# Optimization experiments

Measured on AMD Instinct MI355X. Metric: run time of the kernel, lower is better.

Reference implementation:

```python
import jax, jax.numpy as jnp
import numpy as np

HUGE = 1e31  # ops.HUGE_INT
EPS = 1e-20

NUM_ENT, NUM_REL = 100000, 400
ENT_D, REL_D, HIST_D = 256, 256, 512
ACT_D = ENT_D + REL_D          # 512
IN_D = ENT_D + HIST_D + REL_D  # 1024
B, A = 512, 256


def setup_inputs() -> dict:
    key = jax.random.key(0)
    ks = jax.random.split(key, 10)
    s = 0.02
    return {
        "current_entity": jax.random.randint(ks[0], (B,), 0, NUM_ENT),
        "query_relation": jax.random.randint(ks[1], (B,), 0, NUM_REL),
        "encoded_history": jax.random.normal(ks[2], (B, HIST_D), jnp.float32),
        "r_space": jax.random.randint(ks[3], (B, A), 0, NUM_REL),
        "e_space": jax.random.randint(ks[4], (B, A), 0, NUM_ENT),
        "action_mask": jax.random.randint(ks[5], (B, A), 0, 2).astype(jnp.int32),
        "entity_emb": jax.random.normal(ks[6], (NUM_ENT, ENT_D), jnp.float32) * s,
        "relation_emb": jax.random.normal(ks[7], (NUM_REL, REL_D), jnp.float32) * s,
        "W1": jax.random.normal(ks[8], (IN_D, ACT_D), jnp.float32) * s,
        "b1": jnp.zeros((ACT_D,), jnp.float32),
        "W2": jax.random.normal(ks[9], (ACT_D, ACT_D), jnp.float32) * s,
        "b2": jnp.zeros((ACT_D,), jnp.float32),
    }


def reference(current_entity, query_relation, encoded_history, r_space, e_space,
              action_mask, entity_emb, relation_emb, W1, b1, W2, b2):
    # encode_history: [E(cur) | lstm hidden | R(query)] -> [B, IN_D]
    X = jnp.concatenate([entity_emb[current_entity], encoded_history,
                         relation_emb[query_relation]], axis=-1)
    # policy MLP (dropout = identity in eval)
    X2 = jax.nn.relu(X @ W1 + b1) @ W2 + b2          # [B, ACT_D]
    # per-action embeddings: concat(rel, ent) -> [B, A, ACT_D]
    A_emb = jnp.concatenate([relation_emb[r_space], entity_emb[e_space]], axis=-1)
    mask = action_mask.astype(X2.dtype)
    scores = jnp.einsum('bad,bd->ba', A_emb, X2) - (1.0 - mask) * HUGE
    action_dist = jax.nn.softmax(scores, axis=-1)    # [B, A]
    entropy = -jnp.sum(action_dist * jnp.log(action_dist + EPS), axis=-1)  # [B]
    return action_dist, entropy
```

## Files before the change

### kernel.cpp

```cpp
#include <hip/hip_runtime.h>
#include <hip/hip_bf16.h>

#define ENT_D 256
#define REL_D 256
#define HIST_D 512
#define ACT_DD 512
#define IN_DD 1024
#define BB 512
#define AA 256

typedef short bf16x8 __attribute__((ext_vector_type(8)));
typedef float floatx4 __attribute__((ext_vector_type(4)));

__device__ __forceinline__ unsigned short f2bf(float f) {
    unsigned u = __builtin_bit_cast(unsigned, f);
    return (unsigned short)((u + 0x7fffu + ((u >> 16) & 1u)) >> 16);
}


__global__ __launch_bounds__(256) void pack_kernel(
    const int* __restrict__ cur, const int* __restrict__ qrel,
    const float* __restrict__ hist,
    const float* __restrict__ ent_emb, const float* __restrict__ rel_emb,
    const float* __restrict__ W1, const float* __restrict__ W2,
    unsigned short* __restrict__ W1p, unsigned short* __restrict__ W2p,
    unsigned short* __restrict__ Xp)
{
    const int wid  = blockIdx.x * 4 + (threadIdx.x >> 6);
    const int lane = threadIdx.x & 63;
    const int l15  = lane & 15;
    const int quad = lane >> 4;
    unsigned short v[8];

    if (wid < 1024) {
        const int t = wid, nt = t >> 5, kt = t & 31;
        const int n = nt * 16 + l15, k0 = kt * 32 + quad * 8;
#pragma unroll
        for (int j = 0; j < 8; ++j) v[j] = f2bf(W1[(size_t)(k0 + j) * ACT_DD + n]);
        *(bf16x8*)(W1p + ((size_t)t * 64 + lane) * 8) = *(bf16x8*)v;
    } else if (wid < 1536) {
        const int t = wid - 1024, nt = t >> 4, kt = t & 15;
        const int n = nt * 16 + l15, k0 = kt * 32 + quad * 8;
#pragma unroll
        for (int j = 0; j < 8; ++j) v[j] = f2bf(W2[(size_t)(k0 + j) * ACT_DD + n]);
        *(bf16x8*)(W2p + ((size_t)t * 64 + lane) * 8) = *(bf16x8*)v;
    } else {
        const int t = wid - 1536, mt = t >> 5, kt = t & 31;
        const int m = mt * 16 + l15, k0 = kt * 32 + quad * 8;
        const float* src;
        if (k0 < ENT_D)            src = ent_emb + (size_t)cur[m] * ENT_D + k0;
        else if (k0 < ENT_D + HIST_D) src = hist + (size_t)m * HIST_D + (k0 - ENT_D);
        else                       src = rel_emb + (size_t)qrel[m] * REL_D + (k0 - ENT_D - HIST_D);
        float4 a = *(const float4*)src, b = *(const float4*)(src + 4);
        v[0]=f2bf(a.x); v[1]=f2bf(a.y); v[2]=f2bf(a.z); v[3]=f2bf(a.w);
        v[4]=f2bf(b.x); v[5]=f2bf(b.y); v[6]=f2bf(b.z); v[7]=f2bf(b.w);
        *(bf16x8*)(Xp + ((size_t)t * 64 + lane) * 8) = *(bf16x8*)v;
    }
}

__global__ __launch_bounds__(256) void gemm1_kernel(
    const unsigned short* __restrict__ Xp, const unsigned short* __restrict__ W1p,
    const float* __restrict__ b1, unsigned short* __restrict__ Hp)
{
    __shared__ unsigned short sH[1024];
    const int mt = blockIdx.x, wave = threadIdx.x >> 6, lane = threadIdx.x & 63;
    const int nt = blockIdx.y * 4 + wave;

    const bf16x8* Av = (const bf16x8*)Xp  + (size_t)mt * 32 * 64 + lane;
    const bf16x8* Bv = (const bf16x8*)W1p + (size_t)nt * 32 * 64 + lane;
    floatx4 acc = {0.f, 0.f, 0.f, 0.f};
#pragma unroll 8
    for (int kt = 0; kt < 32; ++kt)
        acc = __builtin_amdgcn_mfma_f32_16x16x32_bf16(Av[kt * 64], Bv[kt * 64], acc, 0, 0, 0);

    const int col  = nt * 16 + (lane & 15);
    const float bj = b1[col];
    const int n_loc = wave * 16 + (lane & 15);
    const int tile_loc = n_loc >> 5, quad2 = (n_loc & 31) >> 3, j2 = n_loc & 7;
#pragma unroll
    for (int reg = 0; reg < 4; ++reg) {
        const int row = (lane >> 4) * 4 + reg;
        const float h = fmaxf(acc[reg] + bj, 0.f);
        sH[tile_loc * 512 + (row + 16 * quad2) * 8 + j2] = f2bf(h);
    }
    __syncthreads();
    const int h = threadIdx.x * 4;
    const int tl = h >> 9, rest = h & 511;
    const size_t dst = ((size_t)(mt * 16 + blockIdx.y * 2 + tl) * 512 + rest);
    *(uint2*)(Hp + dst) = *(const uint2*)(sH + h);
}

__global__ __launch_bounds__(256) void gemm2_kernel(
    const unsigned short* __restrict__ Hp, const unsigned short* __restrict__ W2p,
    const float* __restrict__ b2, float* __restrict__ X2)
{
    const int mt = blockIdx.x, wave = threadIdx.x >> 6, lane = threadIdx.x & 63;
    const int nt = blockIdx.y * 4 + wave;

    const bf16x8* Av = (const bf16x8*)Hp  + (size_t)mt * 16 * 64 + lane;
    const bf16x8* Bv = (const bf16x8*)W2p + (size_t)nt * 16 * 64 + lane;
    floatx4 acc = {0.f, 0.f, 0.f, 0.f};
#pragma unroll
    for (int kt = 0; kt < 16; ++kt)
        acc = __builtin_amdgcn_mfma_f32_16x16x32_bf16(Av[kt * 64], Bv[kt * 64], acc, 0, 0, 0);

    const int col = nt * 16 + (lane & 15);
    const float bj = b2[col];
#pragma unroll
    for (int reg = 0; reg < 4; ++reg) {
        const int m = mt * 16 + (lane >> 4) * 4 + reg;
        X2[(size_t)m * ACT_DD + col] = acc[reg] + bj;
    }
}

__global__ __launch_bounds__(512) void score_softmax_kernel(
    const float* __restrict__ X2,
    const int* __restrict__ r_space, const int* __restrict__ e_space,
    const int* __restrict__ amask,
    const float* __restrict__ ent_emb, const float* __restrict__ rel_emb,
    float* __restrict__ dist, float* __restrict__ ent_out)
{
    __shared__ __align__(16) float x2s[ACT_DD];
    __shared__ float sc[AA];
    __shared__ float red[8];

    const int b = blockIdx.x, tid = threadIdx.x;
    const int wave = tid >> 6, lane = tid & 63;

    x2s[tid] = X2[(size_t)b * ACT_DD + tid];
    __syncthreads();

    const float4 xr = ((const float4*)&x2s[0])[lane];
    const float4 xe = ((const float4*)&x2s[REL_D])[lane];

#pragma unroll
    for (int g = 0; g < 4; ++g) {
        const int ab = wave * 32 + g * 8;
        int ir[8], ie[8];
#pragma unroll
        for (int i = 0; i < 8; ++i) {
            ir[i] = r_space[b * AA + ab + i];
            ie[i] = e_space[b * AA + ab + i];
        }
        float4 r4[8], e4[8];
#pragma unroll
        for (int i = 0; i < 8; ++i)
            r4[i] = ((const float4*)(rel_emb + (size_t)ir[i] * REL_D))[lane];
#pragma unroll
        for (int i = 0; i < 8; ++i)
            e4[i] = ((const float4*)(ent_emb + (size_t)ie[i] * ENT_D))[lane];

        float p[8];
#pragma unroll
        for (int i = 0; i < 8; ++i)
            p[i] = r4[i].x * xr.x + r4[i].y * xr.y + r4[i].z * xr.z + r4[i].w * xr.w
                 + e4[i].x * xe.x + e4[i].y * xe.y + e4[i].z * xe.z + e4[i].w * xe.w;
#pragma unroll
        for (int off = 32; off > 0; off >>= 1) {
#pragma unroll
            for (int i = 0; i < 8; ++i) p[i] += __shfl_xor(p[i], off, 64);
        }
        if (lane == 0) {
#pragma unroll
            for (int i = 0; i < 8; ++i) sc[ab + i] = p[i];
        }
    }
    __syncthreads();

    float s = -3.0e38f;
    if (tid < AA) {
        const float m = (float)amask[b * AA + tid];
        s = sc[tid] - (1.0f - m) * 1e31f;
    }
    float v = s;
#pragma unroll
    for (int off = 32; off > 0; off >>= 1) v = fmaxf(v, __shfl_xor(v, off, 64));
    if (lane == 0) red[wave] = v;
    __syncthreads();
    float mx = red[0];
#pragma unroll
    for (int w = 1; w < 8; ++w) mx = fmaxf(mx, red[w]);
    __syncthreads();

    const float e = (tid < AA) ? __expf(s - mx) : 0.0f;
    v = e;
#pragma unroll
    for (int off = 32; off > 0; off >>= 1) v += __shfl_xor(v, off, 64);
    if (lane == 0) red[wave] = v;
    __syncthreads();
    float sum = red[0];
#pragma unroll
    for (int w = 1; w < 8; ++w) sum += red[w];
    __syncthreads();

    const float p = e / sum;
    if (tid < AA) dist[(size_t)b * AA + tid] = p;

    v = (tid < AA) ? p * __logf(p + 1e-20f) : 0.0f;
#pragma unroll
    for (int off = 32; off > 0; off >>= 1) v += __shfl_xor(v, off, 64);
    if (lane == 0) red[wave] = v;
    __syncthreads();
    if (tid == 0) {
        float t = red[0];
#pragma unroll
        for (int w = 1; w < 8; ++w) t += red[w];
        ent_out[b] = -t;
    }
}

extern "C" void kernel_launch(void* const* d_in, const int* in_sizes, int n_in,
                              void* d_out, int out_size, void* d_ws, size_t ws_size,
                              hipStream_t stream) {
    const int*   cur      = (const int*)d_in[0];
    const int*   qrel     = (const int*)d_in[1];
    const float* hist     = (const float*)d_in[2];
    const int*   r_space  = (const int*)d_in[3];
    const int*   e_space  = (const int*)d_in[4];
    const int*   amask    = (const int*)d_in[5];
    const float* ent_emb  = (const float*)d_in[6];
    const float* rel_emb  = (const float*)d_in[7];
    const float* W1       = (const float*)d_in[8];
    const float* b1       = (const float*)d_in[9];
    const float* W2       = (const float*)d_in[10];
    const float* b2       = (const float*)d_in[11];

    float* dist    = (float*)d_out;
    float* entropy = dist + (size_t)BB * AA;

    char* w = (char*)d_ws;
    unsigned short* W1p = (unsigned short*)(w);
    unsigned short* W2p = (unsigned short*)(w + (1u << 20));
    unsigned short* Xp  = (unsigned short*)(w + (3u << 19));
    unsigned short* Hp  = (unsigned short*)(w + (5u << 19));
    float*          X2  = (float*)(w + (6u << 19));

    pack_kernel<<<640, 256, 0, stream>>>(cur, qrel, hist, ent_emb, rel_emb, W1, W2, W1p, W2p, Xp);
    gemm1_kernel<<<dim3(32, 8), 256, 0, stream>>>(Xp, W1p, b1, Hp);
    gemm2_kernel<<<dim3(32, 8), 256, 0, stream>>>(Hp, W2p, b2, X2);
    score_softmax_kernel<<<512, 512, 0, stream>>>(X2, r_space, e_space, amask,
                                                  ent_emb, rel_emb, dist, entropy);
}
```

Measured before the change: 189.6 us.

## Compact unmasked actions and gather embeddings only for valid actions

Result: faster. 184.8 us (-2.6%).

```diff
diff --git a/kernel.cpp b/kernel.cpp
--- a/kernel.cpp
+++ b/kernel.cpp
@@ -122,25 +122,55 @@
 {
     __shared__ __align__(16) float x2s[ACT_DD];
     __shared__ float sc[AA];
+    __shared__ int   list[AA];
+    __shared__ int   wcnt[4];
+    __shared__ int   n_u_s;
     __shared__ float red[8];
 
     const int b = blockIdx.x, tid = threadIdx.x;
     const int wave = tid >> 6, lane = tid & 63;
 
     x2s[tid] = X2[(size_t)b * ACT_DD + tid];
+
+    int m = 0;
+    unsigned long long bal = 0;
+    int pre = 0;
+    if (tid < AA) {
+        m = amask[b * AA + tid];
+        sc[tid] = 0.0f;
+    }
+    if (wave < 4) {
+        bal = __ballot(m != 0);
+        pre = __popcll(bal & ((1ull << lane) - 1ull));
+        if (lane == 0) wcnt[wave] = __popcll(bal);
+    }
+    __syncthreads();
+
+    if (wave < 4) {
+        int off = 0;
+#pragma unroll
+        for (int w = 0; w < 4; ++w) if (w < wave) off += wcnt[w];
+        if (m != 0) list[off + pre] = tid;
+        if (tid == 0) n_u_s = wcnt[0] + wcnt[1] + wcnt[2] + wcnt[3];
+    }
+    __syncthreads();
+
+    const int n_u = n_u_s;
+    const int padded = (n_u + 63) & ~63;
+    if (tid < padded - n_u) list[n_u + tid] = list[0];
     __syncthreads();
 
     const float4 xr = ((const float4*)&x2s[0])[lane];
     const float4 xe = ((const float4*)&x2s[REL_D])[lane];
 
-#pragma unroll
-    for (int g = 0; g < 4; ++g) {
-        const int ab = wave * 32 + g * 8;
-        int ir[8], ie[8];
+    for (int base = wave * 8; base < padded; base += 64) {
+        int ai[8], ir[8], ie[8];
+#pragma unroll
+        for (int i = 0; i < 8; ++i) ai[i] = list[base + i];
 #pragma unroll
         for (int i = 0; i < 8; ++i) {
-            ir[i] = r_space[b * AA + ab + i];
-            ie[i] = e_space[b * AA + ab + i];
+            ir[i] = r_space[b * AA + ai[i]];
+            ie[i] = e_space[b * AA + ai[i]];
         }
         float4 r4[8], e4[8];
 #pragma unroll
@@ -162,16 +192,13 @@
         }
         if (lane == 0) {
 #pragma unroll
-            for (int i = 0; i < 8; ++i) sc[ab + i] = p[i];
+            for (int i = 0; i < 8; ++i) sc[ai[i]] = p[i];
         }
     }
     __syncthreads();
 
     float s = -3.0e38f;
-    if (tid < AA) {
-        const float m = (float)amask[b * AA + tid];
-        s = sc[tid] - (1.0f - m) * 1e31f;
-    }
+    if (tid < AA) s = (m != 0) ? sc[tid] : (sc[tid] - 1e31f);
     float v = s;
 #pragma unroll
     for (int off = 32; off > 0; off >>= 1) v = fmaxf(v, __shfl_xor(v, off, 64));
```
